# Kernel tuning notes

Measured on AMD Instinct MI355X. Metric: run time of the kernel, lower is better.

Reference implementation:

```python
import jax, jax.numpy as jnp
import numpy as np
import math

DIM = 768
HEADS = 12
HEAD_DIM = DIM // HEADS


def setup_inputs() -> dict:
    key = jax.random.key(0)
    ks = jax.random.split(key, 9)
    s = 1.0 / math.sqrt(DIM)
    x = jax.random.normal(ks[0], (8, 4096, DIM), dtype=jnp.float32)
    Wq = jax.random.normal(ks[1], (DIM, DIM), dtype=jnp.float32) * s
    bq = jnp.zeros((DIM,), dtype=jnp.float32)
    Wk = jax.random.normal(ks[2], (DIM, DIM), dtype=jnp.float32) * s
    bk = jnp.zeros((DIM,), dtype=jnp.float32)
    Wv = jax.random.normal(ks[3], (DIM, DIM), dtype=jnp.float32) * s
    bv = jnp.zeros((DIM,), dtype=jnp.float32)
    Wp = jax.random.normal(ks[4], (DIM, DIM), dtype=jnp.float32) * s
    bp = jnp.zeros((DIM,), dtype=jnp.float32)
    return {"x": x, "Wq": Wq, "bq": bq, "Wk": Wk, "bk": bk,
            "Wv": Wv, "bv": bv, "Wp": Wp, "bp": bp}


def reference(x, Wq, bq, Wk, bk, Wv, bv, Wp, bp):
    B, N, C = x.shape
    H, D = HEADS, HEAD_DIM
    # torch Linear: y = x @ W.T + b
    q = (x @ Wq.T + bq).reshape(B, N, H, D).transpose(0, 2, 1, 3)  # [B,H,N,D]
    k = (x @ Wk.T + bk).reshape(B, N, H, D).transpose(0, 2, 1, 3)
    v = (x @ Wv.T + bv).reshape(B, N, H, D).transpose(0, 2, 1, 3)
    q = jax.nn.softmax(q, axis=-1)   # softmax over head_dim
    k = jax.nn.softmax(k, axis=-2)   # softmax over sequence
    kv = jnp.einsum('bhnd,bhne->bhde', k, v) / math.sqrt(D)  # [B,H,D,D]
    out = jnp.einsum('bhnd,bhde->bhne', q, kv)               # [B,H,N,D]
    out = out.transpose(0, 2, 1, 3).reshape(B, N, C)
    return out @ Wp.T + bp
```

## Files before the change

### kernel.cpp

```cpp
#include <hip/hip_runtime.h>
#include <hip/hip_bf16.h>


#define AS1 __attribute__((address_space(1)))
#define AS3 __attribute__((address_space(3)))

typedef __attribute__((ext_vector_type(8))) short    s16x8;
typedef __attribute__((ext_vector_type(4))) float    f32x4;
typedef __attribute__((ext_vector_type(8))) _Float16 f16x8;
typedef __attribute__((ext_vector_type(4))) unsigned short u16x4;

__device__ __forceinline__ unsigned short f2bf(float f) {
  union { float f; unsigned u; } v; v.f = f;
  unsigned r = v.u + 0x7FFFu + ((v.u >> 16) & 1u);
  return (unsigned short)(r >> 16);
}

__global__ __launch_bounds__(256) void prep(const float* __restrict__ x,
                                            const float* __restrict__ Wq, const float* __restrict__ Wk,
                                            const float* __restrict__ Wv,
                                            const float* __restrict__ bq, const float* __restrict__ bk,
                                            const float* __restrict__ bv,
                                            unsigned short* __restrict__ x_bf,
                                            unsigned short* __restrict__ wqkv_bf,
                                            float* __restrict__ bqkv) {
  const int XB = 2304;
  if ((int)blockIdx.x >= XB) {
    int j = (blockIdx.x - XB) * 256 + threadIdx.x;
    if (j < 768) bqkv[j] = bq[j];
    else if (j < 1536) bqkv[j] = bk[j - 768];
    else if (j < 2304) bqkv[j] = bv[j - 1536];
    return;
  }
  const int n8x = 3145728, n8w = 73728;
  const int stride = XB * 256;
  for (int i = blockIdx.x * 256 + threadIdx.x; i < n8x + 3 * n8w; i += stride) {
    const float* s; unsigned short* d;
    if (i < n8x) { s = x + (size_t)i * 8; d = x_bf + (size_t)i * 8; }
    else {
      int wi = i - n8x, w = wi / n8w, off = wi - w * n8w;
      const float* ws_ = (w == 0) ? Wq : (w == 1) ? Wk : Wv;
      s = ws_ + (size_t)off * 8; d = wqkv_bf + (size_t)wi * 8;
    }
    f32x4 a = ((const f32x4*)s)[0], b = ((const f32x4*)s)[1];
    u16x4 lo, hi;
    lo[0] = f2bf(a[0]); lo[1] = f2bf(a[1]); lo[2] = f2bf(a[2]); lo[3] = f2bf(a[3]);
    hi[0] = f2bf(b[0]); hi[1] = f2bf(b[1]); hi[2] = f2bf(b[2]); hi[3] = f2bf(b[3]);
    ((u16x4*)d)[0] = lo; ((u16x4*)d)[1] = hi;
  }
}

template <int MODE, int BMBLK>
__global__ __launch_bounds__(512, 2) void gemm_rb(const unsigned short* __restrict__ A,
                                                  const unsigned short* __restrict__ Bm,
                                                  const float* __restrict__ bias,
                                                  void* out0, void* out1, void* out2,
                                                  int N, int K, int nb, int batchedB) {
  constexpr int BM = BMBLK * 128;
  constexpr int MI = BMBLK * 4;
  __shared__ unsigned short As[4][BM * 32];
  __shared__ unsigned short Bs[4][256 * 32];
  const int tid = threadIdx.x, lane = tid & 63, wid = tid >> 6;
  const int wr = wid >> 2, wc = wid & 3;
  const int cpx = gridDim.x >> 3;
  const int logical = (blockIdx.x & 7) * cpx + (blockIdx.x >> 3);
  const int m0 = (logical / nb) * BM, n0 = (logical % nb) * 256;
  const unsigned short* Bp = Bm + (batchedB ? ((size_t)(m0 >> 12) * 589824) : 0);

  f32x4 acc[MI][4] = {};
  const int xw = ((tid >> 2) & 3) ^ ((tid >> 4) & 3);
  const int src_off = ((tid & 3) ^ xw) * 8;

  auto stage = [&](int buf, int k0) {
#pragma unroll
    for (int j = 0; j < BMBLK; ++j) {
      int row = j * 128 + (tid >> 2);
      __builtin_amdgcn_global_load_lds(
          (const AS1 void*)(A + (size_t)(m0 + row) * K + k0 + src_off),
          (AS3 void*)(&As[buf][row * 32 + (tid & 3) * 8]), 16, 0, 0);
    }
#pragma unroll
    for (int j = 0; j < 2; ++j) {
      int row = j * 128 + (tid >> 2);
      __builtin_amdgcn_global_load_lds(
          (const AS1 void*)(Bp + (size_t)(n0 + row) * K + k0 + src_off),
          (AS3 void*)(&Bs[buf][row * 32 + (tid & 3) * 8]), 16, 0, 0);
    }
  };

  const int r15 = lane & 15, klog = lane >> 4;
  const int nt = K >> 5;
  stage(0, 0); stage(1, 32); stage(2, 64);

  for (int t = 0; t < nt; ++t) {
    if constexpr (BMBLK == 2) {
      if (t + 3 <= nt)      asm volatile("s_waitcnt vmcnt(8)" ::: "memory");
      else if (t + 2 == nt) asm volatile("s_waitcnt vmcnt(4)" ::: "memory");
      else                  asm volatile("s_waitcnt vmcnt(0)" ::: "memory");
    } else {
      if (t + 3 <= nt)      asm volatile("s_waitcnt vmcnt(6)" ::: "memory");
      else if (t + 2 == nt) asm volatile("s_waitcnt vmcnt(3)" ::: "memory");
      else                  asm volatile("s_waitcnt vmcnt(0)" ::: "memory");
    }
    __builtin_amdgcn_s_barrier();
    if (t + 3 < nt) stage((t + 3) & 3, (t + 3) << 5);

    const unsigned short* Ab = &As[t & 3][0];
    const unsigned short* Bb = &Bs[t & 3][0];
    s16x8 af[MI], bf[4];
#pragma unroll
    for (int i = 0; i < MI; ++i) {
      int row = wr * (BM / 2) + i * 16 + r15;
      int cp = klog ^ ((row & 3) ^ ((row >> 2) & 3));
      af[i] = *(const s16x8*)(Ab + row * 32 + cp * 8);
    }
#pragma unroll
    for (int j = 0; j < 4; ++j) {
      int row = wc * 64 + j * 16 + r15;
      int cp = klog ^ ((row & 3) ^ ((row >> 2) & 3));
      bf[j] = *(const s16x8*)(Bb + row * 32 + cp * 8);
    }
    __builtin_amdgcn_s_setprio(1);
#pragma unroll
    for (int i = 0; i < MI; ++i)
#pragma unroll
      for (int j = 0; j < 4; ++j)
        acc[i][j] = __builtin_amdgcn_mfma_f32_16x16x32_bf16(af[i], bf[j], acc[i][j], 0, 0, 0);
    __builtin_amdgcn_s_setprio(0);
  }

  const int g = lane >> 4, c15 = lane & 15;
  float bj[4];
#pragma unroll
  for (int j = 0; j < 4; ++j) bj[j] = bias[n0 + wc * 64 + j * 16 + c15];

  if (MODE == 0) {
    float* out = (float*)out0;
#pragma unroll
    for (int mi = 0; mi < MI; ++mi)
#pragma unroll
      for (int j = 0; j < 4; ++j) {
        int gr = m0 + wr * (BM / 2) + mi * 16 + g * 4;
        int gc = n0 + wc * 64 + j * 16 + c15;
#pragma unroll
        for (int r = 0; r < 4; ++r)
          out[(size_t)(gr + r) * N + gc] = acc[mi][j][r] + bj[j];
      }
  } else {
    if (n0 < 768) {
      unsigned short* qsm = (unsigned short*)out0;
      const int cbase = n0 + wc * 64;
#pragma unroll
      for (int mi = 0; mi < MI; ++mi) {
#pragma unroll
        for (int r = 0; r < 4; ++r) {
          int gr = m0 + wr * (BM / 2) + mi * 16 + g * 4 + r;
          float v[4];
#pragma unroll
          for (int j = 0; j < 4; ++j) v[j] = acc[mi][j][r] + bj[j];
          float mx = fmaxf(fmaxf(v[0], v[1]), fmaxf(v[2], v[3]));
#pragma unroll
          for (int st = 1; st < 16; st <<= 1) mx = fmaxf(mx, __shfl_xor(mx, st));
          float p[4], sm = 0.f;
#pragma unroll
          for (int j = 0; j < 4; ++j) { p[j] = __expf(v[j] - mx); sm += p[j]; }
#pragma unroll
          for (int st = 1; st < 16; st <<= 1) sm += __shfl_xor(sm, st);
          float inv = 1.0f / sm;
#pragma unroll
          for (int j = 0; j < 4; ++j)
            qsm[(size_t)gr * 768 + cbase + j * 16 + c15] = f2bf(p[j] * inv);
        }
      }
    } else {
      _Float16* dst = (n0 < 1536) ? (_Float16*)out1 : (_Float16*)out2;
      const int cbase = (n0 < 1536 ? n0 - 768 : n0 - 1536) + wc * 64;
#pragma unroll
      for (int mi = 0; mi < MI; ++mi)
#pragma unroll
        for (int j = 0; j < 4; ++j) {
          int gr = m0 + wr * (BM / 2) + mi * 16 + g * 4;
          int cc = cbase + j * 16 + c15;
#pragma unroll
          for (int r = 0; r < 4; ++r)
            dst[(size_t)(gr + r) * 768 + cc] = (_Float16)(acc[mi][j][r] + bj[j]);
        }
    }
  }
}

__global__ __launch_bounds__(256) void kv_partial(const _Float16* __restrict__ kh,
                                                  const _Float16* __restrict__ vh,
                                                  float* __restrict__ kv_part,
                                                  float* __restrict__ z_part) {
  const int bh = blockIdx.x, b = bh / 12, h = bh % 12;
  const int split = blockIdx.y;
  __shared__ float ek_s[64][68];
  __shared__ float v_s[64][68];
  __shared__ float zred[4][64];
  const int t = threadIdx.x;
  const int d0 = (t >> 4) * 4, e0 = (t & 15) * 4;
  const int zd = t & 63, zq = t >> 6;
  float acc[4][4] = {};
  float zp = 0.f;
  const size_t base = (size_t)b * 4096 * 768 + h * 64;

  for (int nc = 0; nc < 8; ++nc) {
    int n0 = split * 512 + nc * 64;
#pragma unroll
    for (int j = 0; j < 2; ++j) {
      int vi = t + j * 256;
      int row = vi >> 3, c8 = (vi & 7) * 8;
      size_t gp = base + (size_t)(n0 + row) * 768 + c8;
      f16x8 k8 = *(const f16x8*)(kh + gp);
      f16x8 v8 = *(const f16x8*)(vh + gp);
      f32x4 e0v, e1v, v0v, v1v;
#pragma unroll
      for (int u = 0; u < 4; ++u) {
        e0v[u] = __expf((float)k8[u]); e1v[u] = __expf((float)k8[4 + u]);
        v0v[u] = (float)v8[u];         v1v[u] = (float)v8[4 + u];
      }
      *(f32x4*)&ek_s[row][c8] = e0v; *(f32x4*)&ek_s[row][c8 + 4] = e1v;
      *(f32x4*)&v_s[row][c8]  = v0v; *(f32x4*)&v_s[row][c8 + 4]  = v1v;
    }
    __syncthreads();
#pragma unroll 4
    for (int r = 0; r < 16; ++r) zp += ek_s[zq * 16 + r][zd];
#pragma unroll 8
    for (int n = 0; n < 64; ++n) {
      f32x4 ekv = *(const f32x4*)&ek_s[n][d0];
      f32x4 vv  = *(const f32x4*)&v_s[n][e0];
#pragma unroll
      for (int i = 0; i < 4; ++i)
#pragma unroll
        for (int j = 0; j < 4; ++j)
          acc[i][j] += ekv[i] * vv[j];
    }
    __syncthreads();
  }
  float* kvp = kv_part + ((size_t)split * 96 + bh) * 4096;
#pragma unroll
  for (int i = 0; i < 4; ++i)
#pragma unroll
    for (int j = 0; j < 4; ++j)
      kvp[(d0 + i) * 64 + e0 + j] = acc[i][j];
  zred[zq][zd] = zp;
  __syncthreads();
  if (t < 64)
    z_part[((size_t)split * 96 + bh) * 64 + t] =
        zred[0][t] + zred[1][t] + zred[2][t] + zred[3][t];
}

__global__ __launch_bounds__(256) void weff_build(const float* __restrict__ kv_part,
                                                  const float* __restrict__ z_part,
                                                  const float* __restrict__ Wp,
                                                  unsigned short* __restrict__ weffT) {
  const int c0 = blockIdx.x * 64, h = blockIdx.y, b = blockIdx.z;
  const int bh = b * 12 + h;
  __shared__ float kvn[64][65];
  __shared__ float zs[64];
  const int t = threadIdx.x;
  if (t < 64) {
    float s = 0.f;
#pragma unroll
    for (int sp = 0; sp < 8; ++sp) s += z_part[((size_t)sp * 96 + bh) * 64 + t];
    zs[t] = s * 8.0f;
  }
  __syncthreads();
#pragma unroll
  for (int i = 0; i < 16; ++i) {
    int idx = t + i * 256;
    int d = idx >> 6;
    float s = 0.f;
#pragma unroll
    for (int sp = 0; sp < 8; ++sp) s += kv_part[((size_t)sp * 96 + bh) * 4096 + idx];
    kvn[d][idx & 63] = s / zs[d];
  }
  __syncthreads();
  const int c = c0 + (t >> 2);
  const int d0 = (t & 3) * 16;
  const float* wrow = Wp + (size_t)c * 768 + h * 64;
  float acc[16] = {};
#pragma unroll 8
  for (int e = 0; e < 64; ++e) {
    float w = wrow[e];
#pragma unroll
    for (int dd = 0; dd < 16; ++dd) acc[dd] += w * kvn[d0 + dd][e];
  }
  unsigned short* orow = weffT + (size_t)b * 589824 + (size_t)c * 768 + h * 64 + d0;
#pragma unroll
  for (int dd = 0; dd < 16; ++dd) orow[dd] = f2bf(acc[dd]);
}

extern "C" void kernel_launch(void* const* d_in, const int* in_sizes, int n_in,
                              void* d_out, int out_size, void* d_ws, size_t ws_size,
                              hipStream_t stream) {
  const float* x  = (const float*)d_in[0];
  const float* Wq = (const float*)d_in[1];
  const float* bq = (const float*)d_in[2];
  const float* Wk = (const float*)d_in[3];
  const float* bk = (const float*)d_in[4];
  const float* Wv = (const float*)d_in[5];
  const float* bv = (const float*)d_in[6];
  const float* Wp = (const float*)d_in[7];
  const float* bp = (const float*)d_in[8];

  const size_t MT = 32768;
  const size_t XE = MT * 768;
  const size_t WE = 768 * 768;

  unsigned short* x_bf    = (unsigned short*)d_ws;
  unsigned short* wqkv_bf = x_bf + XE;
  unsigned short* q_sm    = wqkv_bf + 3 * WE;
  _Float16* k_h = (_Float16*)(q_sm + XE);
  _Float16* v_h = k_h + XE;
  unsigned short* weffT = (unsigned short*)(v_h + XE);
  float* bqkv    = (float*)(weffT + 8 * WE);
  float* kv_part = bqkv + 2304;
  float* z_part  = kv_part + (size_t)8 * 96 * 4096;

  prep<<<2313, 256, 0, stream>>>(x, Wq, Wk, Wv, bq, bk, bv, x_bf, wqkv_bf, bqkv);

  gemm_rb<1, 2><<<1152, 512, 0, stream>>>(x_bf, wqkv_bf, bqkv, q_sm, k_h, v_h, 2304, 768, 9, 0);

  kv_partial<<<dim3(96, 8), 256, 0, stream>>>(k_h, v_h, kv_part, z_part);
  weff_build<<<dim3(12, 12, 8), 256, 0, stream>>>(kv_part, z_part, Wp, weffT);

  gemm_rb<0, 1><<<768, 512, 0, stream>>>(q_sm, weffT, bp, d_out, nullptr, nullptr, 768, 768, 3, 1);
}
```

Before: 380.8 us.

## Replace pipelined 256x256 GEMM with simpler 128x128 single-buffer tile kernel

Swaps the 512-thread, 4-stage multibuffered GEMM (BM up to 256, BN 256, BK 32) for a 256-thread 128x128 tile kernel with BK 64 and a single LDS buffer synced with __syncthreads. Grid sizes quadruple and occupancy target rises to 3 blocks per CU to hide latency through more resident blocks instead of explicit prefetch. The trade-off is less operand reuse per tile and load latency exposed on every k-step, since there is no prefetching.

New measurement: 319.5 us. 16.1% less time.

```diff
diff --git a/kernel.cpp b/kernel.cpp
--- a/kernel.cpp
+++ b/kernel.cpp
@@ -50,98 +50,70 @@
   }
 }
 
-template <int MODE, int BMBLK>
-__global__ __launch_bounds__(512, 2) void gemm_rb(const unsigned short* __restrict__ A,
+template <int MODE>
+__global__ __launch_bounds__(256, 3) void gemm128(const unsigned short* __restrict__ A,
                                                   const unsigned short* __restrict__ Bm,
                                                   const float* __restrict__ bias,
                                                   void* out0, void* out1, void* out2,
                                                   int N, int K, int nb, int batchedB) {
-  constexpr int BM = BMBLK * 128;
-  constexpr int MI = BMBLK * 4;
-  __shared__ unsigned short As[4][BM * 32];
-  __shared__ unsigned short Bs[4][256 * 32];
+  __shared__ unsigned short As[128 * 64];
+  __shared__ unsigned short Bs[128 * 64];
   const int tid = threadIdx.x, lane = tid & 63, wid = tid >> 6;
-  const int wr = wid >> 2, wc = wid & 3;
+  const int wm = wid >> 1, wn = wid & 1;
   const int cpx = gridDim.x >> 3;
   const int logical = (blockIdx.x & 7) * cpx + (blockIdx.x >> 3);
-  const int m0 = (logical / nb) * BM, n0 = (logical % nb) * 256;
+  const int m0 = (logical / nb) * 128, n0 = (logical % nb) * 128;
   const unsigned short* Bp = Bm + (batchedB ? ((size_t)(m0 >> 12) * 589824) : 0);
 
-  f32x4 acc[MI][4] = {};
-  const int xw = ((tid >> 2) & 3) ^ ((tid >> 4) & 3);
-  const int src_off = ((tid & 3) ^ xw) * 8;
-
-  auto stage = [&](int buf, int k0) {
-#pragma unroll
-    for (int j = 0; j < BMBLK; ++j) {
-      int row = j * 128 + (tid >> 2);
+  f32x4 acc[4][4] = {};
+  const int srcc8 = ((tid & 7) ^ ((tid >> 3) & 7)) * 8;
+  const int r15 = lane & 15, hi8 = (lane >> 4) * 8, sw = (lane & 7) * 8;
+
+  const int nt = K >> 6;
+  for (int t = 0; t < nt; ++t) {
+    const int k0 = t << 6;
+#pragma unroll
+    for (int j = 0; j < 4; ++j) {
+      int row = j * 32 + (tid >> 3);
       __builtin_amdgcn_global_load_lds(
-          (const AS1 void*)(A + (size_t)(m0 + row) * K + k0 + src_off),
-          (AS3 void*)(&As[buf][row * 32 + (tid & 3) * 8]), 16, 0, 0);
-    }
-#pragma unroll
-    for (int j = 0; j < 2; ++j) {
-      int row = j * 128 + (tid >> 2);
+          (const AS1 void*)(A + (size_t)(m0 + row) * K + k0 + srcc8),
+          (AS3 void*)(&As[row * 64 + (tid & 7) * 8]), 16, 0, 0);
       __builtin_amdgcn_global_load_lds(
-          (const AS1 void*)(Bp + (size_t)(n0 + row) * K + k0 + src_off),
-          (AS3 void*)(&Bs[buf][row * 32 + (tid & 3) * 8]), 16, 0, 0);
-    }
-  };
-
-  const int r15 = lane & 15, klog = lane >> 4;
-  const int nt = K >> 5;
-  stage(0, 0); stage(1, 32); stage(2, 64);
-
-  for (int t = 0; t < nt; ++t) {
-    if constexpr (BMBLK == 2) {
-      if (t + 3 <= nt)      asm volatile("s_waitcnt vmcnt(8)" ::: "memory");
-      else if (t + 2 == nt) asm volatile("s_waitcnt vmcnt(4)" ::: "memory");
-      else                  asm volatile("s_waitcnt vmcnt(0)" ::: "memory");
-    } else {
-      if (t + 3 <= nt)      asm volatile("s_waitcnt vmcnt(6)" ::: "memory");
-      else if (t + 2 == nt) asm volatile("s_waitcnt vmcnt(3)" ::: "memory");
-      else                  asm volatile("s_waitcnt vmcnt(0)" ::: "memory");
-    }
-    __builtin_amdgcn_s_barrier();
-    if (t + 3 < nt) stage((t + 3) & 3, (t + 3) << 5);
-
-    const unsigned short* Ab = &As[t & 3][0];
-    const unsigned short* Bb = &Bs[t & 3][0];
-    s16x8 af[MI], bf[4];
-#pragma unroll
-    for (int i = 0; i < MI; ++i) {
-      int row = wr * (BM / 2) + i * 16 + r15;
-      int cp = klog ^ ((row & 3) ^ ((row >> 2) & 3));
-      af[i] = *(const s16x8*)(Ab + row * 32 + cp * 8);
-    }
-#pragma unroll
-    for (int j = 0; j < 4; ++j) {
-      int row = wc * 64 + j * 16 + r15;
-      int cp = klog ^ ((row & 3) ^ ((row >> 2) & 3));
-      bf[j] = *(const s16x8*)(Bb + row * 32 + cp * 8);
-    }
-    __builtin_amdgcn_s_setprio(1);
-#pragma unroll
-    for (int i = 0; i < MI; ++i)
+          (const AS1 void*)(Bp + (size_t)(n0 + row) * K + k0 + srcc8),
+          (AS3 void*)(&Bs[row * 64 + (tid & 7) * 8]), 16, 0, 0);
+    }
+    __syncthreads();
+#pragma unroll
+    for (int kk = 0; kk < 2; ++kk) {
+      s16x8 af[4], bf[4];
+#pragma unroll
+      for (int i = 0; i < 4; ++i)
+        af[i] = *(const s16x8*)(As + (wm * 64 + i * 16 + r15) * 64 + ((kk * 32 + hi8) ^ sw));
 #pragma unroll
       for (int j = 0; j < 4; ++j)
-        acc[i][j] = __builtin_amdgcn_mfma_f32_16x16x32_bf16(af[i], bf[j], acc[i][j], 0, 0, 0);
-    __builtin_amdgcn_s_setprio(0);
+        bf[j] = *(const s16x8*)(Bs + (wn * 64 + j * 16 + r15) * 64 + ((kk * 32 + hi8) ^ sw));
+#pragma unroll
+      for (int i = 0; i < 4; ++i)
+#pragma unroll
+        for (int j = 0; j < 4; ++j)
+          acc[i][j] = __builtin_amdgcn_mfma_f32_16x16x32_bf16(af[i], bf[j], acc[i][j], 0, 0, 0);
+    }
+    __syncthreads();
   }
 
   const int g = lane >> 4, c15 = lane & 15;
   float bj[4];
 #pragma unroll
-  for (int j = 0; j < 4; ++j) bj[j] = bias[n0 + wc * 64 + j * 16 + c15];
+  for (int j = 0; j < 4; ++j) bj[j] = bias[n0 + wn * 64 + j * 16 + c15];
 
   if (MODE == 0) {
     float* out = (float*)out0;
 #pragma unroll
-    for (int mi = 0; mi < MI; ++mi)
+    for (int mi = 0; mi < 4; ++mi)
 #pragma unroll
       for (int j = 0; j < 4; ++j) {
-        int gr = m0 + wr * (BM / 2) + mi * 16 + g * 4;
-        int gc = n0 + wc * 64 + j * 16 + c15;
+        int gr = m0 + wm * 64 + mi * 16 + g * 4;
+        int gc = n0 + wn * 64 + j * 16 + c15;
 #pragma unroll
         for (int r = 0; r < 4; ++r)
           out[(size_t)(gr + r) * N + gc] = acc[mi][j][r] + bj[j];
@@ -149,12 +121,12 @@
   } else {
     if (n0 < 768) {
       unsigned short* qsm = (unsigned short*)out0;
-      const int cbase = n0 + wc * 64;
-#pragma unroll
-      for (int mi = 0; mi < MI; ++mi) {
+      const int cbase = n0 + wn * 64;
+#pragma unroll
+      for (int mi = 0; mi < 4; ++mi) {
 #pragma unroll
         for (int r = 0; r < 4; ++r) {
-          int gr = m0 + wr * (BM / 2) + mi * 16 + g * 4 + r;
+          int gr = m0 + wm * 64 + mi * 16 + g * 4 + r;
           float v[4];
 #pragma unroll
           for (int j = 0; j < 4; ++j) v[j] = acc[mi][j][r] + bj[j];
@@ -174,12 +146,12 @@
       }
     } else {
       _Float16* dst = (n0 < 1536) ? (_Float16*)out1 : (_Float16*)out2;
-      const int cbase = (n0 < 1536 ? n0 - 768 : n0 - 1536) + wc * 64;
-#pragma unroll
-      for (int mi = 0; mi < MI; ++mi)
+      const int cbase = (n0 < 1536 ? n0 - 768 : n0 - 1536) + wn * 64;
+#pragma unroll
+      for (int mi = 0; mi < 4; ++mi)
 #pragma unroll
         for (int j = 0; j < 4; ++j) {
-          int gr = m0 + wr * (BM / 2) + mi * 16 + g * 4;
+          int gr = m0 + wm * 64 + mi * 16 + g * 4;
           int cc = cbase + j * 16 + c15;
 #pragma unroll
           for (int r = 0; r < 4; ++r)
@@ -321,10 +293,10 @@
 
   prep<<<2313, 256, 0, stream>>>(x, Wq, Wk, Wv, bq, bk, bv, x_bf, wqkv_bf, bqkv);
 
-  gemm_rb<1, 2><<<1152, 512, 0, stream>>>(x_bf, wqkv_bf, bqkv, q_sm, k_h, v_h, 2304, 768, 9, 0);
+  gemm128<1><<<4608, 256, 0, stream>>>(x_bf, wqkv_bf, bqkv, q_sm, k_h, v_h, 2304, 768, 18, 0);
 
   kv_partial<<<dim3(96, 8), 256, 0, stream>>>(k_h, v_h, kv_part, z_part);
   weff_build<<<dim3(12, 12, 8), 256, 0, stream>>>(kv_part, z_part, Wp, weffT);
 
-  gemm_rb<0, 1><<<768, 512, 0, stream>>>(q_sm, weffT, bp, d_out, nullptr, nullptr, 768, 768, 3, 1);
-}
+  gemm128<0><<<1536, 256, 0, stream>>>(q_sm, weffT, bp, d_out, nullptr, nullptr, 768, 768, 6, 1);
+}
```
